# Kernel optimization log

Measured on AMD Instinct MI355X. Metric: run time of the kernel, lower is better.

The kernel has to match this reference:

```python
import jax, jax.numpy as jnp
from jax import lax
import numpy as np

B, T, N, C = 8, 12, 80, 12
HID, KS, KC = 32, 3, 2
OUT_HORIZON = 6
ALPHA = 3.0


def _xavier(key, shape):
    std = np.sqrt(2.0 / (shape[0] + shape[-1])).astype(np.float32)
    return jax.random.normal(key, shape, dtype=jnp.float32) * std


def setup_inputs():
    key = jax.random.key(0)
    ks = jax.random.split(key, 20)
    N2, C2 = N * N, C * C
    d_enc = (1 + HID) * KS * KC   # gates/candi input dim for encoder cell (input_dim=1)
    d_dec = (2 * HID) * KS * KC   # decoder cell input dim (output_dim=hidden)
    As = jax.random.uniform(ks[1], (N, N), dtype=jnp.float32)
    Ac = jax.random.uniform(ks[2], (C, C), dtype=jnp.float32)
    return dict(
        X_seq=jax.random.normal(ks[0], (B, T, N, C), dtype=jnp.float32),
        As=As / As.sum(-1, keepdims=True),   # row-stochastic graph for stable Chebyshev
        Ac=Ac / Ac.sum(-1, keepdims=True),
        WuS=_xavier(ks[3], (C, HID)), WvS=_xavier(ks[4], (C, HID)),
        WuC=_xavier(ks[5], (N, HID)), WvC=_xavier(ks[6], (N, HID)),
        WA_S=_xavier(ks[7], (N2, N2)), bA_S=jnp.zeros((N2,), jnp.float32),
        WP_S=_xavier(ks[8], (N2, N2)), bP_S=jnp.zeros((N2,), jnp.float32),
        WA_C=_xavier(ks[9], (C2, C2)), bA_C=jnp.zeros((C2,), jnp.float32),
        WP_C=_xavier(ks[10], (C2, C2)), bP_C=jnp.zeros((C2,), jnp.float32),
        enc_Wg=_xavier(ks[11], (d_enc, 2 * HID)), enc_bg=jnp.zeros((2 * HID,), jnp.float32),
        enc_Wc=_xavier(ks[12], (d_enc, HID)), enc_bc=jnp.zeros((HID,), jnp.float32),
        dec_Wg=_xavier(ks[13], (d_dec, 2 * HID)), dec_bg=jnp.zeros((2 * HID,), jnp.float32),
        dec_Wc=_xavier(ks[14], (d_dec, HID)), dec_bc=jnp.zeros((HID,), jnp.float32),
        W1=_xavier(ks[15], (HID, HID // 2)), b1=jnp.zeros((HID // 2,), jnp.float32),
        W2=_xavier(ks[16], (HID // 2, 1)), b2=jnp.zeros((1,), jnp.float32),
    )


def _mixed_fusion(A, P, WA, bA, WP, bP):
    n = A.shape[0]
    a = jax.nn.sigmoid(A.reshape(-1) @ WA + bA + P.reshape(-1) @ WP + bP).reshape(n, n)
    return a * A + (1.0 - a) * P


def _mgp(X, As, Ac, WuS, WvS, WuC, WvC, WA_S, bA_S, WP_S, bP_S, WA_C, bA_C, WP_C, bP_C):
    # X: [B,T,N,C]
    Us = jnp.tanh(ALPHA * (X @ WuS))           # [B,T,N,h]
    Vs = jnp.tanh(ALPHA * (X @ WvS))
    M = jnp.einsum('btnh,btmh->nm', Us, Vs)
    Ps = jax.nn.softmax(jax.nn.relu(M - M.T), axis=-1)
    Gs = _mixed_fusion(As, Ps, WA_S, bA_S, WP_S, bP_S)
    Xc = jnp.swapaxes(X, 2, 3)                 # [B,T,C,N]
    Uc = jnp.tanh(ALPHA * (Xc @ WuC))
    Vc = jnp.tanh(ALPHA * (Xc @ WvC))
    Mc = jnp.einsum('btnh,btmh->nm', Uc, Vc)
    Pc = jax.nn.softmax(jax.nn.relu(Mc - Mc.T), axis=-1)
    Gc = _mixed_fusion(Ac, Pc, WA_C, bA_C, WP_C, bP_C)
    return Gs, Gc


def _cheby(G, K):
    Gset = [jnp.eye(G.shape[0], dtype=G.dtype), G]
    for _ in range(2, K):
        Gset.append(2.0 * (G @ Gset[-1]) - Gset[-2])
    return Gset[:K]


def _bdg(X, Gs_set, Gc_set, W, b):
    # X: [B,N,C,D]; Chebyshev bidirectional diffusion: mode-1 then mode-2 products
    feats = []
    for Gn in Gs_set:
        Xn = jnp.einsum('bncl,nm->bmcl', X, Gn)
        for Gk in Gc_set:
            feats.append(jnp.einsum('bmcl,cd->bmdl', Xn, Gk))
    feat = jnp.concatenate(feats, axis=-1)     # [B,N,C,D*Ks*Kc]
    return jnp.einsum('bmdk,kh->bmdh', feat, W) + b


def _cell(Gs_set, Gc_set, Xt, H, Wg, bg, Wc, bc):
    XH = jnp.concatenate([Xt, H], axis=-1)
    g = _bdg(XH, Gs_set, Gc_set, Wg, bg)
    update = jax.nn.sigmoid(g[..., :HID])
    reset = jax.nn.sigmoid(g[..., HID:])
    cand = jnp.tanh(_bdg(jnp.concatenate([Xt, reset * H], axis=-1), Gs_set, Gc_set, Wc, bc))
    return (1.0 - update) * H + update * cand


def _forward(X_seq, As, Ac, WuS, WvS, WuC, WvC, WA_S, bA_S, WP_S, bP_S,
             WA_C, bA_C, WP_C, bP_C, enc_Wg, enc_bg, enc_Wc, enc_bc,
             dec_Wg, dec_bg, dec_Wc, dec_bc, W1, b1, W2, b2):
    Gs, Gc = _mgp(X_seq, As, Ac, WuS, WvS, WuC, WvC,
                  WA_S, bA_S, WP_S, bP_S, WA_C, bA_C, WP_C, bP_C)
    Gs_set = _cheby(Gs, KS)
    Gc_set = _cheby(Gc, KC)
    X5 = X_seq[..., None]                       # [B,T,N,C,1]

    def step(H, Xt):
        Hn = _cell(Gs_set, Gc_set, Xt, H, enc_Wg, enc_bg, enc_Wc, enc_bc)
        return Hn, None

    H0 = jnp.zeros((X_seq.shape[0], N, C, HID), dtype=X_seq.dtype)
    Hend, _ = lax.scan(step, H0, jnp.swapaxes(X5, 0, 1))  # scan over T

    # decoder: GRU cell fed with its own hidden, out_proj per step
    H_dec, Xin = Hend, Hend
    outs = []
    for _ in range(OUT_HORIZON):
        H_dec = _cell(Gs_set, Gc_set, Xin, H_dec, dec_Wg, dec_bg, dec_Wc, dec_bc)
        outs.append((jnp.tanh(0.0) + (H_dec @ W1 + b1)) @ W2 + b2)
        Xin = H_dec
    return jnp.stack(outs, axis=1)[..., 0]      # [B,out_horizon,N,C]


def reference(X_seq, As, Ac, WuS, WvS, WuC, WvC, WA_S, bA_S, WP_S, bP_S,
              WA_C, bA_C, WP_C, bP_C, enc_Wg, enc_bg, enc_Wc, enc_bc,
              dec_Wg, dec_bg, dec_Wc, dec_bc, W1, b1, W2, b2):
    return _forward(X_seq, As, Ac, WuS, WvS, WuC, WvC, WA_S, bA_S, WP_S, bP_S,
                    WA_C, bA_C, WP_C, bP_C, enc_Wg, enc_bg, enc_Wc, enc_bc,
                    dec_Wg, dec_bg, dec_Wc, dec_bc, W1, b1, W2, b2)
```

## Files before the change

kernel.cpp:

```cpp
#include <hip/hip_runtime.h>
#include <hip/hip_bf16.h>


__global__ void k_pack(const float* __restrict__ eWg, const float* __restrict__ eWc,
                       const float* __restrict__ dWg, const float* __restrict__ dWc,
                       const float* __restrict__ W1, const float* __restrict__ b1,
                       const float* __restrict__ W2, const float* __restrict__ b2,
                       float* encWgh, float* encWch, float* WgX, float* WcX,
                       float* decWgc, float* decWcx, float* decWch, float* w12, float* c0) {
  int t = threadIdx.x;
  for (int idx = t; idx < 192*64; idx += 256) {
    int row = idx / 64, hh = idx % 64; int f = row / 32, ll = row % 32;
    encWgh[idx] = eWg[(f*33 + 1 + ll)*64 + hh];
    decWgc[idx] = dWg[(f*64 + ll)*64 + hh] + dWg[(f*64 + 32 + ll)*64 + hh];
  }
  for (int idx = t; idx < 192*32; idx += 256) {
    int row = idx / 32, hh = idx % 32; int f = row / 32, ll = row % 32;
    encWch[idx] = eWc[(f*33 + 1 + ll)*32 + hh];
    decWcx[idx] = dWc[(f*64 + ll)*32 + hh];
    decWch[idx] = dWc[(f*64 + 32 + ll)*32 + hh];
  }
  for (int idx = t; idx < 384; idx += 256) { int f = idx/64, hh = idx%64; WgX[idx] = eWg[(f*33)*64 + hh]; }
  if (t < 192) { int f = t/32, hh = t%32; WcX[t] = eWc[(f*33)*32 + hh]; }
  if (t < 32) { float s = 0; for (int j = 0; j < 16; ++j) s += W1[t*16+j]*W2[j]; w12[t] = s; }
  if (t == 0) { float s = 0; for (int j = 0; j < 16; ++j) s += b1[j]*W2[j]; c0[0] = s + b2[0]; }
}

__global__ __launch_bounds__(256) void k_uv(const float* __restrict__ X,
                                            const float* __restrict__ WuS, const float* __restrict__ WvS,
                                            const float* __restrict__ WuC, const float* __restrict__ WvC,
                                            float* __restrict__ Us, float* __restrict__ Vs,
                                            float* __restrict__ Uc, float* __restrict__ Vc) {
  int t = threadIdx.x;
  int h = t & 31;
  if (blockIdx.x < 960) {
    int row = blockIdx.x*8 + (t >> 5);
    const float* xr = X + (size_t)row*12;
    float su = 0.f, sv = 0.f;
#pragma unroll
    for (int c = 0; c < 12; ++c) {
      float x = xr[c];
      su += x*WuS[c*32+h]; sv += x*WvS[c*32+h];
    }
    Us[(size_t)row*32 + h] = tanhf(3.f*su);
    Vs[(size_t)row*32 + h] = tanhf(3.f*sv);
  } else {
    int row = (blockIdx.x - 960)*8 + (t >> 5);
    int bt = row / 12, c = row % 12;
    const float* xb = X + (size_t)bt*960 + c;
    float su = 0.f, sv = 0.f;
    for (int n = 0; n < 80; ++n) {
      float x = xb[n*12];
      su += x*WuC[n*32+h]; sv += x*WvC[n*32+h];
    }
    Uc[(size_t)row*32 + h] = tanhf(3.f*su);
    Vc[(size_t)row*32 + h] = tanhf(3.f*sv);
  }
}

__global__ __launch_bounds__(256) void k_m_mc(const float* __restrict__ Us, const float* __restrict__ Vs,
                                              const float* __restrict__ Uc, const float* __restrict__ Vc,
                                              float* __restrict__ M, float* __restrict__ Mc) {
  __shared__ float su[8][16][33], sv[8][16][33];
  int t = threadIdx.x;
  if (blockIdx.x < 25) {
    int m0 = (blockIdx.x % 5)*16, n0 = (blockIdx.x / 5)*16;
    int tx = t & 15, ty = t >> 4;
    float acc = 0.f;
    for (int r0 = 0; r0 < 96; r0 += 8) {
      for (int idx = t; idx < 8*16*32; idx += 256) {
        int hh = idx & 31, i = (idx >> 5) & 15, rr = idx >> 9;
        su[rr][i][hh] = Us[((size_t)(r0+rr)*80 + n0 + i)*32 + hh];
        sv[rr][i][hh] = Vs[((size_t)(r0+rr)*80 + m0 + i)*32 + hh];
      }
      __syncthreads();
      for (int rr = 0; rr < 8; ++rr) {
#pragma unroll
        for (int hh = 0; hh < 32; ++hh) acc += su[rr][ty][hh] * sv[rr][tx][hh];
      }
      __syncthreads();
    }
    M[(n0+ty)*80 + (m0+tx)] = acc;
  } else {
    if (t < 144) {
      int c1 = t / 12, c2 = t % 12;
      float acc = 0.f;
      for (int r = 0; r < 96; ++r)
        for (int hh = 0; hh < 32; ++hh)
          acc += Uc[((size_t)r*12+c1)*32+hh] * Vc[((size_t)r*12+c2)*32+hh];
      Mc[t] = acc;
    }
  }
}

__global__ void k_softmax2(const float* __restrict__ Ms, float* __restrict__ Ps,
                           const float* __restrict__ Mc, float* __restrict__ Pc) {
  int lane = threadIdx.x;
  const float* M; float* P; int row, n;
  if (blockIdx.x < 80) { M = Ms; P = Ps; row = blockIdx.x; n = 80; }
  else                 { M = Mc; P = Pc; row = blockIdx.x - 80; n = 12; }
  float v0 = -1e30f, v1 = -1e30f;
  {
    int m = lane;
    if (m < n) { float a = M[row*n + m] - M[m*n + row]; v0 = a > 0.f ? a : 0.f; }
    m = 64 + lane;
    if (m < n) { float a = M[row*n + m] - M[m*n + row]; v1 = a > 0.f ? a : 0.f; }
  }
  float mx = fmaxf(v0, v1);
  for (int off = 32; off; off >>= 1) mx = fmaxf(mx, __shfl_xor(mx, off));
  float s = 0.f;
  if (lane < n)      { v0 = expf(v0 - mx); s += v0; }
  if (64 + lane < n) { v1 = expf(v1 - mx); s += v1; }
  for (int off = 32; off; off >>= 1) s += __shfl_xor(s, off);
  float inv = 1.f / s;
  if (lane < n)      P[row*n + lane] = v0 * inv;
  if (64 + lane < n) P[row*n + 64 + lane] = v1 * inv;
}

__global__ __launch_bounds__(128) void k_fus_partial(
    const float* __restrict__ A, const float* __restrict__ P,
    const float* __restrict__ WA, const float* __restrict__ WP,
    float* __restrict__ part) {
  int lane = threadIdx.x, sub = threadIdx.y;
  int jb = (blockIdx.x + blockIdx.y) % 25;
  int chunk = blockIdx.y;
  int j = jb*256 + lane*4;
  int i0 = chunk*50 + sub*25;
  float4 acc = {0.f, 0.f, 0.f, 0.f};
  for (int ii = 0; ii < 25; ii += 5) {
    float a[5], p[5]; float4 wa[5], wp[5];
#pragma unroll
    for (int u = 0; u < 5; ++u) {
      int i = i0 + ii + u;
      a[u] = A[i]; p[u] = P[i];
      wa[u] = *(const float4*)(WA + (size_t)i*6400 + j);
      wp[u] = *(const float4*)(WP + (size_t)i*6400 + j);
    }
#pragma unroll
    for (int u = 0; u < 5; ++u) {
      acc.x += a[u]*wa[u].x + p[u]*wp[u].x;
      acc.y += a[u]*wa[u].y + p[u]*wp[u].y;
      acc.z += a[u]*wa[u].z + p[u]*wp[u].z;
      acc.w += a[u]*wa[u].w + p[u]*wp[u].w;
    }
  }
  __shared__ float4 red[2][64];
  red[sub][lane] = acc;
  __syncthreads();
  if (sub == 0) {
    float4 r0 = red[0][lane], r1 = red[1][lane];
    float4 o = {r0.x+r1.x, r0.y+r1.y, r0.z+r1.z, r0.w+r1.w};
    *(float4*)(part + (size_t)chunk*6400 + j) = o;
  }
}

__global__ void k_final2(const float* __restrict__ part,
                         const float* __restrict__ bA, const float* __restrict__ bP,
                         const float* __restrict__ A, const float* __restrict__ P,
                         float* __restrict__ G,
                         const float* __restrict__ Ac, const float* __restrict__ Pc,
                         const float* __restrict__ WA_C, const float* __restrict__ WP_C,
                         const float* __restrict__ bA_C, const float* __restrict__ bP_C,
                         float* __restrict__ Gc) {
  int t = threadIdx.x;
  if (blockIdx.x < 25) {
    int j = blockIdx.x*256 + t;
    float s = 0.f;
    for (int k = 0; k < 128; ++k) s += part[(size_t)k*6400 + j];
    s += bA[j] + bP[j];
    float a = 1.f / (1.f + expf(-s));
    G[j] = a*A[j] + (1.f - a)*P[j];
  } else if (t < 144) {
    float s = 0.f;
    for (int i = 0; i < 144; ++i) s += Ac[i]*WA_C[i*144+t] + Pc[i]*WP_C[i*144+t];
    s += bA_C[t] + bP_C[t];
    float a = 1.f / (1.f + expf(-s));
    Gc[t] = a*Ac[t] + (1.f - a)*Pc[t];
  }
}

__global__ void k_cheby(const float* __restrict__ G, float* __restrict__ G2) {
  int j = blockIdx.x*256 + threadIdx.x;
  int n = j / 80, m = j % 80;
  float s = 0.f;
  for (int k = 0; k < 80; ++k) s += G[n*80+k]*G[k*80+m];
  G2[j] = 2.f*s - (n == m ? 1.f : 0.f);
}

__global__ __launch_bounds__(256) void k_gx(const float* __restrict__ X,
                                            const float* __restrict__ Gs, const float* __restrict__ Gs2,
                                            const float* __restrict__ Gc,
                                            const float* __restrict__ WgX, const float* __restrict__ WcX,
                                            float* __restrict__ gXg, float* __restrict__ gXc,
                                            float* __restrict__ Hz) {
  int bt = blockIdx.x, q = blockIdx.y, t = threadIdx.x;
  for (int i = (bt*4 + q)*256 + t; i < 245760; i += 98304) Hz[i] = 0.f;
  __shared__ float xl[960], xg1[240], xg2[240], S[240*6];
  for (int i = t; i < 960; i += 256) xl[i] = X[(size_t)bt*960 + i];
  __syncthreads();
  if (t < 240) {
    int nl = t / 12, c = t % 12, n = q*20 + nl;
    float s1 = 0.f, s2 = 0.f;
    for (int np = 0; np < 80; ++np) { float x = xl[np*12 + c]; s1 += Gs[np*80+n]*x; s2 += Gs2[np*80+n]*x; }
    xg1[t] = s1; xg2[t] = s2;
    S[t*6+0] = xl[n*12+c]; S[t*6+2] = s1; S[t*6+4] = s2;
  }
  __syncthreads();
  if (t < 240) {
    int nl = t / 12, c = t % 12, n = q*20 + nl;
    float a1 = 0.f, a3 = 0.f, a5 = 0.f;
    for (int cp = 0; cp < 12; ++cp) {
      float g = Gc[cp*12 + c];
      a1 += xl[n*12+cp]*g; a3 += xg1[nl*12+cp]*g; a5 += xg2[nl*12+cp]*g;
    }
    S[t*6+1] = a1; S[t*6+3] = a3; S[t*6+5] = a5;
  }
  __syncthreads();
  for (int idx = t; idx < 240*64; idx += 256) {
    int h = idx % 64, pair = idx / 64; int nl = pair/12, c = pair%12; int n = q*20+nl;
    float s = 0.f;
#pragma unroll
    for (int f = 0; f < 6; ++f) s += S[pair*6+f] * WgX[f*64+h];
    gXg[((size_t)bt*960 + n*12 + c)*64 + h] = s;
  }
  for (int idx = t; idx < 240*32; idx += 256) {
    int h = idx % 32, pair = idx / 32; int nl = pair/12, c = pair%12; int n = q*20+nl;
    float s = 0.f;
#pragma unroll
    for (int f = 0; f < 6; ++f) s += S[pair*6+f] * WcX[f*32+h];
    gXc[((size_t)bt*960 + n*12 + c)*32 + h] = s;
  }
}

__global__ __launch_bounds__(256) void k_cell0(const float* __restrict__ gXg,
                                               const float* __restrict__ gXc,
                                               const float* __restrict__ ebg,
                                               const float* __restrict__ ebc,
                                               float* __restrict__ H) {
  int idx = blockIdx.x*256 + threadIdx.x;
  int b = idx / 30720, rem = idx % 30720;
  int pos = rem / 32, h = rem % 32;
  float gu = gXg[((size_t)(b*12)*960 + pos)*64 + h] + ebg[h];
  float gc = gXc[((size_t)(b*12)*960 + pos)*32 + h] + ebc[h];
  float u = 1.f / (1.f + expf(-gu));
  H[idx] = u * tanhf(gc);
}

template<int HOUT, int MODE, bool HAS_U2, bool HAS_FIELD, bool DO_PROJ>
__global__ __launch_bounds__(256) void k_cell(
    const float* __restrict__ U1, const float* __restrict__ W1p,
    const float* __restrict__ U2, const float* __restrict__ W2p,
    const float* __restrict__ field, int fbs,
    const float* __restrict__ bias,
    const float* __restrict__ Gsd, const float* __restrict__ Gs2d, const float* __restrict__ Gcd,
    const float* Hbuf, const float* updbuf,
    float* outA, float* outB,
    const float* __restrict__ w12p, const float* __restrict__ c0p,
    float* projp, int step)
{
  constexpr int MT = 2;
  constexpr int NG = 256 / HOUT;
  constexpr int NP = (MT*12) / NG;
  const int t = threadIdx.x;
  const int b = blockIdx.y;
  const int m0 = blockIdx.x * MT;
  __shared__ float fA[3*MT*384];
  __shared__ float fB[3*MT*384];
  const int mg = t >> 7;
  const int u  = t & 127;
  const int c0 = u >> 5;
  const int l  = u & 31;
  const int h  = t % HOUT;
  const int pg = t / HOUT;
  int bofs[NP];
#pragma unroll
  for (int p = 0; p < NP; ++p) bofs[p] = (p*NG + pg) * 32;
  float outr[NP];
#pragma unroll
  for (int p = 0; p < NP; ++p) outr[p] = 0.f;

  const size_t ub_base = (size_t)b*80*12*32;
  const int nrounds = HAS_U2 ? 2 : 1;
  for (int rnd = 0; rnd < nrounds; ++rnd) {
    const float* U  = rnd ? U2 : U1;
    const float* Wp = rnd ? W2p : W1p;
    if (rnd) __syncthreads();
    float a0[3], a1[3], a2[3];
#pragma unroll
    for (int j = 0; j < 3; ++j) { a1[j] = 0.f; a2[j] = 0.f; }
    const float* Ub = U + ub_base;
    for (int n = 0; n < 80; ++n) {
      float g1 = Gsd[n*80 + m0 + mg];
      float g2 = Gs2d[n*80 + m0 + mg];
#pragma unroll
      for (int j = 0; j < 3; ++j) {
        float x = Ub[(n*12 + c0 + 4*j)*32 + l];
        a1[j] += g1*x; a2[j] += g2*x;
      }
    }
#pragma unroll
    for (int j = 0; j < 3; ++j) a0[j] = Ub[((m0+mg)*12 + c0 + 4*j)*32 + l];
#pragma unroll
    for (int j = 0; j < 3; ++j) {
      int cc = c0 + 4*j;
      fA[(0*MT+mg)*384 + cc*32 + l] = a0[j];
      fA[(1*MT+mg)*384 + cc*32 + l] = a1[j];
      fA[(2*MT+mg)*384 + cc*32 + l] = a2[j];
    }
    __syncthreads();
    for (int idx = t; idx < 3*MT*384; idx += 256) {
      int ll = idx & 31;
      int d  = (idx >> 5) % 12;
      int km = idx / 384;
      float s = 0.f;
#pragma unroll
      for (int c = 0; c < 12; ++c) s += fA[km*384 + c*32 + ll] * Gcd[c*12 + d];
      fB[km*384 + d*32 + ll] = s;
    }
    __syncthreads();
    for (int f = 0; f < 6; ++f) {
      int kn = f >> 1;
      const float* src = ((f & 1) ? fB : fA) + kn*MT*384;
#pragma unroll
      for (int l4 = 0; l4 < 8; ++l4) {
        const float w0 = Wp[(f*32 + l4*4 + 0)*HOUT + h];
        const float w1 = Wp[(f*32 + l4*4 + 1)*HOUT + h];
        const float w2 = Wp[(f*32 + l4*4 + 2)*HOUT + h];
        const float w3 = Wp[(f*32 + l4*4 + 3)*HOUT + h];
#pragma unroll
        for (int p = 0; p < NP; ++p) {
          const float4 v = *(const float4*)&src[bofs[p] + l4*4];
          outr[p] += v.x*w0 + v.y*w1 + v.z*w2 + v.w*w3;
        }
      }
    }
  }
#pragma unroll
  for (int p = 0; p < NP; ++p) {
    int pair = p*NG + pg;
    int m = pair / 12, c = pair % 12;
    int n = m0 + m;
    size_t oidx = (size_t)(b*80 + n)*12 + c;
    float g = outr[p] + bias[h];
    if (HAS_FIELD) g += field[(size_t)b*fbs + (size_t)(n*12 + c)*HOUT + h];
    if (MODE == 0) {
      float sg = 1.f / (1.f + expf(-g));
      size_t hb = oidx*32;
      if (h < 32) outA[hb + h] = sg;
      else        outB[hb + (h-32)] = sg * Hbuf[hb + (h-32)];
    } else {
      float cd = tanhf(g);
      size_t hi = oidx*32 + h;
      float uu = updbuf[hi];
      float hv = Hbuf[hi];
      float hn = (1.f - uu)*hv + uu*cd;
      outA[hi] = hn;
      if (DO_PROJ) {
        float pv = hn * w12p[h];
        for (int off = 16; off; off >>= 1) pv += __shfl_down(pv, off, 32);
        if (h == 0) projp[((size_t)(b*6 + step)*80 + n)*12 + c] = pv + c0p[0];
      }
    }
  }
}

extern "C" void kernel_launch(void* const* d_in, const int* in_sizes, int n_in,
                              void* d_out, int out_size, void* d_ws, size_t ws_size,
                              hipStream_t stream) {
  (void)in_sizes; (void)n_in; (void)out_size;
  const float* X    = (const float*)d_in[0];
  const float* As   = (const float*)d_in[1];
  const float* Ac   = (const float*)d_in[2];
  const float* WuS  = (const float*)d_in[3];
  const float* WvS  = (const float*)d_in[4];
  const float* WuC  = (const float*)d_in[5];
  const float* WvC  = (const float*)d_in[6];
  const float* WA_S = (const float*)d_in[7];
  const float* bA_S = (const float*)d_in[8];
  const float* WP_S = (const float*)d_in[9];
  const float* bP_S = (const float*)d_in[10];
  const float* WA_C = (const float*)d_in[11];
  const float* bA_C = (const float*)d_in[12];
  const float* WP_C = (const float*)d_in[13];
  const float* bP_C = (const float*)d_in[14];
  const float* eWg  = (const float*)d_in[15];
  const float* ebg  = (const float*)d_in[16];
  const float* eWc  = (const float*)d_in[17];
  const float* ebc  = (const float*)d_in[18];
  const float* dWg  = (const float*)d_in[19];
  const float* dbg  = (const float*)d_in[20];
  const float* dWc  = (const float*)d_in[21];
  const float* dbc  = (const float*)d_in[22];
  const float* W1   = (const float*)d_in[23];
  const float* b1   = (const float*)d_in[24];
  const float* W2   = (const float*)d_in[25];
  const float* b2   = (const float*)d_in[26];
  float* out = (float*)d_out;

  float* w = (float*)d_ws;
  size_t o = 0;
  auto alloc = [&](size_t n) { float* p = w + o; o += (n + 63) & ~(size_t)63; return p; };
  float* Us     = alloc(245760);
  float* Vs     = alloc(245760);
  float* Uc     = alloc(36864);
  float* Vc     = alloc(36864);
  float* Mb     = alloc(6400);
  float* Mc     = alloc(144);
  float* Ps     = alloc(6400);
  float* Pc     = alloc(144);
  float* part   = alloc((size_t)128*6400);
  float* Gs     = alloc(6400);
  float* Gc     = alloc(144);
  float* Gs2    = alloc(6400);
  float* encWgh = alloc(192*64);
  float* encWch = alloc(192*32);
  float* WgX    = alloc(384);
  float* WcX    = alloc(192);
  float* decWgc = alloc(192*64);
  float* decWcx = alloc(192*32);
  float* decWch = alloc(192*32);
  float* w12    = alloc(32);
  float* c0     = alloc(64);
  float* H      = alloc(245760);
  float* H2     = alloc(245760);
  float* upd    = alloc(245760);
  float* rH     = alloc(245760);
  float* gXg    = alloc((size_t)5898240);
  float* gXc    = alloc((size_t)2949120);
  if (o * sizeof(float) > ws_size) return;

  k_pack<<<1,256,0,stream>>>(eWg, eWc, dWg, dWc, W1, b1, W2, b2,
                             encWgh, encWch, WgX, WcX, decWgc, decWcx, decWch, w12, c0);
  k_uv<<<1104,256,0,stream>>>(X, WuS, WvS, WuC, WvC, Us, Vs, Uc, Vc);
  k_m_mc<<<26,256,0,stream>>>(Us, Vs, Uc, Vc, Mb, Mc);
  k_softmax2<<<92,64,0,stream>>>(Mb, Ps, Mc, Pc);
  k_fus_partial<<<dim3(25,128),dim3(64,2),0,stream>>>(As, Ps, WA_S, WP_S, part);
  k_final2<<<26,256,0,stream>>>(part, bA_S, bP_S, As, Ps, Gs,
                                Ac, Pc, WA_C, WP_C, bA_C, bP_C, Gc);
  k_cheby<<<25,256,0,stream>>>(Gs, Gs2);
  k_gx<<<dim3(96,4),256,0,stream>>>(X, Gs, Gs2, Gc, WgX, WcX, gXg, gXc, H);

  k_cell0<<<960,256,0,stream>>>(gXg, gXc, ebg, ebc, H);

  for (int t = 1; t < 12; ++t) {
    k_cell<64,0,false,true,false><<<dim3(40,8),256,0,stream>>>(
        H, encWgh, nullptr, nullptr, gXg + (size_t)t*61440, 737280, ebg,
        Gs, Gs2, Gc, H, nullptr, upd, rH, nullptr, nullptr, nullptr, 0);
    k_cell<32,1,false,true,false><<<dim3(40,8),256,0,stream>>>(
        rH, encWch, nullptr, nullptr, gXc + (size_t)t*30720, 368640, ebc,
        Gs, Gs2, Gc, H, upd, H, nullptr, nullptr, nullptr, nullptr, 0);
  }
  float* Hd = H; float* Hn = H2;
  for (int i = 0; i < 6; ++i) {
    k_cell<64,0,false,false,false><<<dim3(40,8),256,0,stream>>>(
        Hd, decWgc, nullptr, nullptr, nullptr, 0, dbg,
        Gs, Gs2, Gc, Hd, nullptr, upd, rH, nullptr, nullptr, nullptr, 0);
    k_cell<32,1,true,false,true><<<dim3(40,8),256,0,stream>>>(
        Hd, decWcx, rH, decWch, nullptr, 0, dbc,
        Gs, Gs2, Gc, Hd, upd, Hn, nullptr, w12, c0, out, i);
    float* tmp = Hd; Hd = Hn; Hn = tmp;
  }
}
```

Measured before the change: 1.068 ms.

## Split graph-conv reduction across thread halves and restructure fusion partial GEMV

The recurrent cell kernel now launches 512 threads per block. Two halves each reduce 40 of the 80 graph nodes and combine their partial sums through shared memory, and the projection is spread over more threads. The fusion GEMV is reorganised so each of 400 blocks owns 16 input rows and covers all 6400 outputs with 320 threads. This gives fully coalesced streaming of the large weight matrices, but it quadruples the partial buffer that k_final2 must reduce serially.

```diff
diff --git a/kernel.cpp b/kernel.cpp
--- a/kernel.cpp
+++ b/kernel.cpp
@@ -117,41 +117,39 @@
   if (64 + lane < n) P[row*n + 64 + lane] = v1 * inv;
 }
 
-__global__ __launch_bounds__(128) void k_fus_partial(
+__global__ __launch_bounds__(320) void k_fus_partial(
     const float* __restrict__ A, const float* __restrict__ P,
     const float* __restrict__ WA, const float* __restrict__ WP,
     float* __restrict__ part) {
-  int lane = threadIdx.x, sub = threadIdx.y;
-  int jb = (blockIdx.x + blockIdx.y) % 25;
-  int chunk = blockIdx.y;
-  int j = jb*256 + lane*4;
-  int i0 = chunk*50 + sub*25;
-  float4 acc = {0.f, 0.f, 0.f, 0.f};
-  for (int ii = 0; ii < 25; ii += 5) {
-    float a[5], p[5]; float4 wa[5], wp[5];
-#pragma unroll
-    for (int u = 0; u < 5; ++u) {
-      int i = i0 + ii + u;
-      a[u] = A[i]; p[u] = P[i];
-      wa[u] = *(const float4*)(WA + (size_t)i*6400 + j);
-      wp[u] = *(const float4*)(WP + (size_t)i*6400 + j);
-    }
-#pragma unroll
-    for (int u = 0; u < 5; ++u) {
-      acc.x += a[u]*wa[u].x + p[u]*wp[u].x;
-      acc.y += a[u]*wa[u].y + p[u]*wp[u].y;
-      acc.z += a[u]*wa[u].z + p[u]*wp[u].z;
-      acc.w += a[u]*wa[u].w + p[u]*wp[u].w;
-    }
-  }
-  __shared__ float4 red[2][64];
-  red[sub][lane] = acc;
-  __syncthreads();
-  if (sub == 0) {
-    float4 r0 = red[0][lane], r1 = red[1][lane];
-    float4 o = {r0.x+r1.x, r0.y+r1.y, r0.z+r1.z, r0.w+r1.w};
-    *(float4*)(part + (size_t)chunk*6400 + j) = o;
-  }
+  const int t = threadIdx.x;
+  const int chunk = blockIdx.x;
+  float4 acc[5];
+#pragma unroll
+  for (int q = 0; q < 5; ++q) acc[q] = make_float4(0.f, 0.f, 0.f, 0.f);
+  const int i0 = chunk*16;
+  for (int r = 0; r < 16; ++r) {
+    const int i = i0 + r;
+    const float a = A[i], p = P[i];
+    const float* wa = WA + (size_t)i*6400;
+    const float* wp = WP + (size_t)i*6400;
+    float4 va[5], vp[5];
+#pragma unroll
+    for (int q = 0; q < 5; ++q) {
+      const int j = t*4 + q*1280;
+      va[q] = *(const float4*)(wa + j);
+      vp[q] = *(const float4*)(wp + j);
+    }
+#pragma unroll
+    for (int q = 0; q < 5; ++q) {
+      acc[q].x += a*va[q].x + p*vp[q].x;
+      acc[q].y += a*va[q].y + p*vp[q].y;
+      acc[q].z += a*va[q].z + p*vp[q].z;
+      acc[q].w += a*va[q].w + p*vp[q].w;
+    }
+  }
+  float* po = part + (size_t)chunk*6400;
+#pragma unroll
+  for (int q = 0; q < 5; ++q) *(float4*)(po + t*4 + q*1280) = acc[q];
 }
 
 __global__ void k_final2(const float* __restrict__ part,
@@ -166,7 +164,7 @@
   if (blockIdx.x < 25) {
     int j = blockIdx.x*256 + t;
     float s = 0.f;
-    for (int k = 0; k < 128; ++k) s += part[(size_t)k*6400 + j];
+    for (int k = 0; k < 400; ++k) s += part[(size_t)k*6400 + j];
     s += bA[j] + bP[j];
     float a = 1.f / (1.f + expf(-s));
     G[j] = a*A[j] + (1.f - a)*P[j];
@@ -247,7 +245,7 @@
 }
 
 template<int HOUT, int MODE, bool HAS_U2, bool HAS_FIELD, bool DO_PROJ>
-__global__ __launch_bounds__(256) void k_cell(
+__global__ __launch_bounds__(512) void k_cell(
     const float* __restrict__ U1, const float* __restrict__ W1p,
     const float* __restrict__ U2, const float* __restrict__ W2p,
     const float* __restrict__ field, int fbs,
@@ -258,23 +256,22 @@
     const float* __restrict__ w12p, const float* __restrict__ c0p,
     float* projp, int step)
 {
-  constexpr int MT = 2;
-  constexpr int NG = 256 / HOUT;
-  constexpr int NP = (MT*12) / NG;
+  __shared__ float fA[2304];
+  __shared__ float fB[2304];
+  __shared__ float fP[1536];
   const int t = threadIdx.x;
   const int b = blockIdx.y;
-  const int m0 = blockIdx.x * MT;
-  __shared__ float fA[3*MT*384];
-  __shared__ float fB[3*MT*384];
-  const int mg = t >> 7;
-  const int u  = t & 127;
+  const int m0 = blockIdx.x * 2;
+  const int nh = t >> 8;
+  const int r8 = t & 255;
+  const int mg = r8 >> 7;
+  const int u  = r8 & 127;
   const int c0 = u >> 5;
   const int l  = u & 31;
+  constexpr int NG = 512 / HOUT;
+  constexpr int NP = (HOUT == 64) ? 3 : 2;
   const int h  = t % HOUT;
   const int pg = t / HOUT;
-  int bofs[NP];
-#pragma unroll
-  for (int p = 0; p < NP; ++p) bofs[p] = (p*NG + pg) * 32;
   float outr[NP];
 #pragma unroll
   for (int p = 0; p < NP; ++p) outr[p] = 0.f;
@@ -285,30 +282,40 @@
     const float* U  = rnd ? U2 : U1;
     const float* Wp = rnd ? W2p : W1p;
     if (rnd) __syncthreads();
-    float a0[3], a1[3], a2[3];
-#pragma unroll
-    for (int j = 0; j < 3; ++j) { a1[j] = 0.f; a2[j] = 0.f; }
-    const float* Ub = U + ub_base;
-    for (int n = 0; n < 80; ++n) {
-      float g1 = Gsd[n*80 + m0 + mg];
-      float g2 = Gs2d[n*80 + m0 + mg];
-#pragma unroll
-      for (int j = 0; j < 3; ++j) {
-        float x = Ub[(n*12 + c0 + 4*j)*32 + l];
-        a1[j] += g1*x; a2[j] += g2*x;
-      }
-    }
-#pragma unroll
-    for (int j = 0; j < 3; ++j) a0[j] = Ub[((m0+mg)*12 + c0 + 4*j)*32 + l];
-#pragma unroll
-    for (int j = 0; j < 3; ++j) {
-      int cc = c0 + 4*j;
-      fA[(0*MT+mg)*384 + cc*32 + l] = a0[j];
-      fA[(1*MT+mg)*384 + cc*32 + l] = a1[j];
-      fA[(2*MT+mg)*384 + cc*32 + l] = a2[j];
+    {
+      float a1[3] = {0.f,0.f,0.f}, a2[3] = {0.f,0.f,0.f};
+      const float* Ub = U + ub_base;
+      const int nbeg = nh*40;
+      for (int n = nbeg; n < nbeg + 40; ++n) {
+        float g1 = Gsd[n*80 + m0 + mg];
+        float g2 = Gs2d[n*80 + m0 + mg];
+#pragma unroll
+        for (int j = 0; j < 3; ++j) {
+          float x = Ub[(n*12 + c0 + 4*j)*32 + l];
+          a1[j] += g1*x; a2[j] += g2*x;
+        }
+      }
+      if (nh == 0) {
+#pragma unroll
+        for (int j = 0; j < 3; ++j) {
+          int cc = c0 + 4*j;
+          fA[(0 + mg)*384 + cc*32 + l] = Ub[((m0+mg)*12 + cc)*32 + l];
+          fA[(2 + mg)*384 + cc*32 + l] = a1[j];
+          fA[(4 + mg)*384 + cc*32 + l] = a2[j];
+        }
+      } else {
+#pragma unroll
+        for (int j = 0; j < 3; ++j) {
+          int cc = c0 + 4*j;
+          fP[(0 + mg)*384 + cc*32 + l] = a1[j];
+          fP[(2 + mg)*384 + cc*32 + l] = a2[j];
+        }
+      }
     }
     __syncthreads();
-    for (int idx = t; idx < 3*MT*384; idx += 256) {
+    for (int idx = t; idx < 1536; idx += 512) fA[768 + idx] += fP[idx];
+    __syncthreads();
+    for (int idx = t; idx < 2304; idx += 512) {
       int ll = idx & 31;
       int d  = (idx >> 5) % 12;
       int km = idx / 384;
@@ -320,7 +327,7 @@
     __syncthreads();
     for (int f = 0; f < 6; ++f) {
       int kn = f >> 1;
-      const float* src = ((f & 1) ? fB : fA) + kn*MT*384;
+      const float* src = ((f & 1) ? fB : fA) + kn*768;
 #pragma unroll
       for (int l4 = 0; l4 < 8; ++l4) {
         const float w0 = Wp[(f*32 + l4*4 + 0)*HOUT + h];
@@ -329,8 +336,11 @@
         const float w3 = Wp[(f*32 + l4*4 + 3)*HOUT + h];
 #pragma unroll
         for (int p = 0; p < NP; ++p) {
-          const float4 v = *(const float4*)&src[bofs[p] + l4*4];
-          outr[p] += v.x*w0 + v.y*w1 + v.z*w2 + v.w*w3;
+          int pair = p*NG + pg;
+          if (pair < 24) {
+            const float4 v = *(const float4*)&src[pair*32 + l4*4];
+            outr[p] += v.x*w0 + v.y*w1 + v.z*w2 + v.w*w3;
+          }
         }
       }
     }
@@ -338,6 +348,7 @@
 #pragma unroll
   for (int p = 0; p < NP; ++p) {
     int pair = p*NG + pg;
+    if (pair >= 24) break;
     int m = pair / 12, c = pair % 12;
     int n = m0 + m;
     size_t oidx = (size_t)(b*80 + n)*12 + c;
@@ -408,7 +419,7 @@
   float* Mc     = alloc(144);
   float* Ps     = alloc(6400);
   float* Pc     = alloc(144);
-  float* part   = alloc((size_t)128*6400);
+  float* part   = alloc((size_t)400*6400);
   float* Gs     = alloc(6400);
   float* Gc     = alloc(144);
   float* Gs2    = alloc(6400);
@@ -434,7 +445,7 @@
   k_uv<<<1104,256,0,stream>>>(X, WuS, WvS, WuC, WvC, Us, Vs, Uc, Vc);
   k_m_mc<<<26,256,0,stream>>>(Us, Vs, Uc, Vc, Mb, Mc);
   k_softmax2<<<92,64,0,stream>>>(Mb, Ps, Mc, Pc);
-  k_fus_partial<<<dim3(25,128),dim3(64,2),0,stream>>>(As, Ps, WA_S, WP_S, part);
+  k_fus_partial<<<400,320,0,stream>>>(As, Ps, WA_S, WP_S, part);
   k_final2<<<26,256,0,stream>>>(part, bA_S, bP_S, As, Ps, Gs,
                                 Ac, Pc, WA_C, WP_C, bA_C, bP_C, Gc);
   k_cheby<<<25,256,0,stream>>>(Gs, Gs2);
@@ -443,19 +454,19 @@
   k_cell0<<<960,256,0,stream>>>(gXg, gXc, ebg, ebc, H);
 
   for (int t = 1; t < 12; ++t) {
-    k_cell<64,0,false,true,false><<<dim3(40,8),256,0,stream>>>(
+    k_cell<64,0,false,true,false><<<dim3(40,8),512,0,stream>>>(
         H, encWgh, nullptr, nullptr, gXg + (size_t)t*61440, 737280, ebg,
         Gs, Gs2, Gc, H, nullptr, upd, rH, nullptr, nullptr, nullptr, 0);
-    k_cell<32,1,false,true,false><<<dim3(40,8),256,0,stream>>>(
+    k_cell<32,1,false,true,false><<<dim3(40,8),512,0,stream>>>(
         rH, encWch, nullptr, nullptr, gXc + (size_t)t*30720, 368640, ebc,
         Gs, Gs2, Gc, H, upd, H, nullptr, nullptr, nullptr, nullptr, 0);
   }
   float* Hd = H; float* Hn = H2;
   for (int i = 0; i < 6; ++i) {
-    k_cell<64,0,false,false,false><<<dim3(40,8),256,0,stream>>>(
+    k_cell<64,0,false,false,false><<<dim3(40,8),512,0,stream>>>(
         Hd, decWgc, nullptr, nullptr, nullptr, 0, dbg,
         Gs, Gs2, Gc, Hd, nullptr, upd, rH, nullptr, nullptr, nullptr, 0);
-    k_cell<32,1,true,false,true><<<dim3(40,8),256,0,stream>>>(
+    k_cell<32,1,true,false,true><<<dim3(40,8),512,0,stream>>>(
         Hd, decWcx, rH, decWch, nullptr, 0, dbc,
         Gs, Gs2, Gc, Hd, upd, Hn, nullptr, w12, c0, out, i);
     float* tmp = Hd; Hd = Hn; Hn = tmp;
```

New measurement: 1.082 ms. No clear change (+1.3%).
